# Optimization experiments

Measured on AMD Instinct MI355X. Metric: run time of the kernel, lower is better.

Reference implementation:

```python
import jax, jax.numpy as jnp
import numpy as np

DIM = 64
IN_CH = 3 * DIM          # 192
HID_CH = 2 * IN_CH       # 384
BN_EPS = 1e-5


def setup_inputs() -> dict:
    key = jax.random.key(0)
    ks = jax.random.split(key, 6)
    B, H, W = 8, 256, 256
    x = jax.random.normal(ks[0], (B, H, W, DIM), dtype=jnp.float32)
    gamma = jnp.ones((IN_CH,), dtype=jnp.float32)
    beta = jnp.zeros((IN_CH,), dtype=jnp.float32)
    w_in = jax.random.normal(ks[1], (HID_CH, IN_CH), dtype=jnp.float32) * (1.0 / np.sqrt(IN_CH))
    w_dw = jax.random.normal(ks[2], (HID_CH, 1, 3, 3), dtype=jnp.float32) * (1.0 / 3.0)
    w_out = jax.random.normal(ks[3], (IN_CH, HID_CH), dtype=jnp.float32) * (1.0 / np.sqrt(HID_CH))
    res_scale = jnp.ones((1,), dtype=jnp.float32)
    return {"x": x, "gamma": gamma, "beta": beta, "w_in": w_in,
            "w_dw": w_dw, "w_out": w_out, "res_scale": res_scale}


def _dwt(xc):
    # xc: (B, C, H, W) NCHW, H and W even. Haar via strided slices.
    B, C, H, W = xc.shape
    a = xc[:, :, 0::2, 0::2]
    b = xc[:, :, 0::2, 1::2]
    c = xc[:, :, 1::2, 0::2]
    d = xc[:, :, 1::2, 1::2]
    LLc = (a + b + c + d) * 0.5
    LHc = (a - b + c - d) * 0.5
    HLc = (a + b - c - d) * 0.5
    HHc = (a - b - c + d) * 0.5
    # torch grouped conv output channel order is (channel, subband) flattened,
    # then chunk(4) splits contiguously -> each chunk mixes subbands. Replicate.
    y = jnp.stack([LLc, LHc, HLc, HHc], axis=2)        # (B, C, 4, h, w)
    y = y.reshape(B, 4 * C, H // 2, W // 2)
    return y[:, 0*C:1*C], y[:, 1*C:2*C], y[:, 2*C:3*C], y[:, 3*C:4*C]


def _iwt(LL, LH, HL, HH):
    B, C, h, w = LL.shape
    # cat along channels then view(B,4,C,h,w): interprets as (4, C) layout.
    x4 = jnp.concatenate([LL, LH, HL, HH], axis=1).reshape(B, 4, C, h, w)
    # out[b,c,2p+r,2q+s] = x4[b, 2r+s, c, p, q]
    arr = x4.transpose(0, 2, 1, 3, 4).reshape(B, C, 2, 2, h, w)
    out = arr.transpose(0, 1, 4, 2, 5, 3).reshape(B, C, 2 * h, 2 * w)
    return out


def _mlp(high, gamma, beta, w_in, w_dw, w_out, res_scale):
    # BatchNorm2d in training mode: biased batch stats over (B, H, W)
    mean = jnp.mean(high, axis=(0, 2, 3))
    var = jnp.var(high, axis=(0, 2, 3))
    xn = (high - mean[None, :, None, None]) * jax.lax.rsqrt(var + BN_EPS)[None, :, None, None]
    xn = xn * gamma[None, :, None, None] + beta[None, :, None, None]
    h = jnp.einsum('oc,bchw->bohw', w_in, xn)           # 1x1 conv, no bias
    h = jax.lax.conv_general_dilated(
        h, w_dw, window_strides=(1, 1), padding=((1, 1), (1, 1)),
        dimension_numbers=('NCHW', 'OIHW', 'NCHW'),
        feature_group_count=HID_CH)                      # depthwise 3x3
    h = jax.nn.gelu(h, approximate=False)                # torch nn.GELU default: exact erf
    h = jnp.einsum('oc,bchw->bohw', w_out, h)            # 1x1 conv, no bias
    return high + res_scale[0] * h


def reference(x, gamma, beta, w_in, w_dw, w_out, res_scale):
    xc = jnp.transpose(x, (0, 3, 1, 2))                  # NHWC -> NCHW
    LL, LH, HL, HH = _dwt(xc)
    high = jnp.concatenate([LH, HL, HH], axis=1)         # (B, 3C, h, w)
    high_enh = _mlp(high, gamma, beta, w_in, w_dw, w_out, res_scale)
    C = LL.shape[1]
    LHo, HLo, HHo = high_enh[:, :C], high_enh[:, C:2*C], high_enh[:, 2*C:]
    out = _iwt(LL, LHo, HLo, HHo)                        # (B, C, H, W)
    return jnp.transpose(out, (0, 2, 3, 1))              # back to NHWC
```

## Files before the change

### kernel.cpp

```cpp
#include <hip/hip_runtime.h>
#include <math.h>

typedef unsigned short u16;
typedef unsigned int u32;
typedef __attribute__((ext_vector_type(4))) float f4;
typedef __attribute__((ext_vector_type(2))) float f2;
typedef __attribute__((ext_vector_type(4))) u16 u16x4;
typedef __attribute__((ext_vector_type(8))) u16 u16x8;
typedef __attribute__((ext_vector_type(8))) short bf8;

#define N_IMG 8
#define HS 128
#define NPOS (N_IMG*HS*HS)
#define IN_CH 192
#define HID_CH 384

__device__ __forceinline__ u16 f2bf(float f) {
  union { float f; u32 u; } v; v.f = f;
  u32 r = v.u + 0x7FFFu + ((v.u >> 16) & 1u);
  return (u16)(r >> 16);
}
__device__ __forceinline__ float bf2f(u16 u) {
  union { u32 u; float f; } v; v.u = ((u32)u) << 16; return v.f;
}
__device__ __forceinline__ f2 bfpair(u32 d) {
  union { u32 u; float f; } lo, hi;
  lo.u = d << 16; hi.u = d & 0xffff0000u;
  f2 r; r[0] = lo.f; r[1] = hi.f; return r;
}
__device__ __forceinline__ float gelu_fast(float x) {
  float x2 = x * x;
  float z = x * (-2.302208f - 0.102942f * x2);
  float e = __builtin_amdgcn_exp2f(z);
  return x * __builtin_amdgcn_rcpf(1.0f + e);
}
__device__ __forceinline__ void gl_lds16(const u16* g, u16* l) {
  __builtin_amdgcn_global_load_lds(
      (__attribute__((address_space(1))) void*)(u16*)g,
      (__attribute__((address_space(3))) void*)l, 16, 0, 0);
}

__global__ void k0_zero(float* stats) { stats[threadIdx.x] = 0.0f; }

__global__ __launch_bounds__(256) void k1_dwt(
    const float* __restrict__ x,
    u16* __restrict__ high,
    float* __restrict__ out,
    float* __restrict__ stats)
{
  const int blk = blockIdx.x;
  const int b = blk >> 8, i = (blk >> 1) & 127, jh = blk & 1;
  const int t = threadIdx.x;
  const int c4 = t & 15;
  const int j0 = t >> 4;
  const int jbase = jh * 64 + j0;
  const int rowE = ((b * 256 + 2 * i) * 256) * 64;
  const int rowO = rowE + 256 * 64;
  const bool isHigh = (c4 >= 4);

  float sacc[16], qacc[16];
#pragma unroll
  for (int v = 0; v < 16; v++) { sacc[v] = 0.f; qacc[v] = 0.f; }

  f4 R[2][4];
  {
    const int colE = (2 * jbase) * 64 + c4 * 4;
    R[0][0] = *(const f4*)(x + rowE + colE);
    R[0][1] = *(const f4*)(x + rowE + colE + 64);
    R[0][2] = *(const f4*)(x + rowO + colE);
    R[0][3] = *(const f4*)(x + rowO + colE + 64);
  }

#pragma unroll
  for (int iter = 0; iter < 4; ++iter) {
    const int cur = iter & 1, nxt = cur ^ 1;
    if (iter < 3) {
      const int jn = jbase + 16 * (iter + 1);
      const int colE = (2 * jn) * 64 + c4 * 4;
      R[nxt][0] = *(const f4*)(x + rowE + colE);
      R[nxt][1] = *(const f4*)(x + rowE + colE + 64);
      R[nxt][2] = *(const f4*)(x + rowO + colE);
      R[nxt][3] = *(const f4*)(x + rowO + colE + 64);
    }
    const int j = jbase + 16 * iter;
    f4 va = R[cur][0], vb = R[cur][1], vc = R[cur][2], vd = R[cur][3];
    f4 sb0 = (va + vb + vc + vd) * 0.5f;
    f4 sb1 = (va - vb + vc - vd) * 0.5f;
    f4 sb2 = (va + vb - vc - vd) * 0.5f;
    f4 sb3 = (va - vb - vc + vd) * 0.5f;

    if (!isHigh) {
      float* dst = out + rowE + (2 * j) * 64 + 16 * c4;
#pragma unroll
      for (int cc = 0; cc < 4; cc++) {
        f4 ov;
        ov[0] = sb0[cc]; ov[1] = sb1[cc]; ov[2] = sb2[cc]; ov[3] = sb3[cc];
        ((f4*)dst)[cc] = ov;
      }
    } else {
      const int n = b * 16384 + i * 128 + j;
      u16* dst = high + n * 192 + 16 * (c4 - 4);
#pragma unroll
      for (int half = 0; half < 2; half++) {
        u16x8 pk;
#pragma unroll
        for (int cc2 = 0; cc2 < 2; cc2++) {
          const int cc = half * 2 + cc2;
          pk[cc2 * 4 + 0] = f2bf(sb0[cc]);
          pk[cc2 * 4 + 1] = f2bf(sb1[cc]);
          pk[cc2 * 4 + 2] = f2bf(sb2[cc]);
          pk[cc2 * 4 + 3] = f2bf(sb3[cc]);
        }
        *(u16x8*)(dst + half * 8) = pk;
      }
#pragma unroll
      for (int cc = 0; cc < 4; cc++) {
        float e0 = sb0[cc], e1 = sb1[cc], e2 = sb2[cc], e3 = sb3[cc];
        sacc[cc * 4 + 0] += e0; qacc[cc * 4 + 0] += e0 * e0;
        sacc[cc * 4 + 1] += e1; qacc[cc * 4 + 1] += e1 * e1;
        sacc[cc * 4 + 2] += e2; qacc[cc * 4 + 2] += e2 * e2;
        sacc[cc * 4 + 3] += e3; qacc[cc * 4 + 3] += e3 * e3;
      }
    }
  }

  float vals[32];
#pragma unroll
  for (int v = 0; v < 16; v++) { vals[v] = sacc[v]; vals[16 + v] = qacc[v]; }
#pragma unroll
  for (int v = 0; v < 32; v++) {
    float xx = vals[v];
    xx += __shfl_down(xx, 32);
    xx += __shfl_down(xx, 16);
    vals[v] = xx;
  }
  __shared__ float sred[4][12][32];
  const int lane = t & 63, wave = t >> 6;
  if (lane >= 4 && lane < 16) {
#pragma unroll
    for (int v = 0; v < 32; v++) sred[wave][lane - 4][v] = vals[v];
  }
  __syncthreads();
  if (t < 192) {
    const int g = t >> 4, L = t & 15;
    float s = sred[0][g][L] + sred[1][g][L] + sred[2][g][L] + sred[3][g][L];
    float q = sred[0][g][16 + L] + sred[1][g][16 + L] + sred[2][g][16 + L] + sred[3][g][16 + L];
    atomicAdd(&stats[t], s);
    atomicAdd(&stats[192 + t], q);
  }
}

__global__ void k2a(const float* __restrict__ stats, const float* __restrict__ gamma,
                    const float* __restrict__ beta, float* __restrict__ st)
{
  const int t = threadIdx.x;
  if (t < 192) {
    const float inv_n = 1.0f / 131072.0f;
    float mean = stats[t] * inv_n;
    float var = stats[192 + t] * inv_n - mean * mean;
    var = fmaxf(var, 0.0f);
    float s = gamma[t] * rsqrtf(var + 1e-5f);
    st[t] = s;
    st[192 + t] = beta[t] - mean * s;
  }
}

__global__ __launch_bounds__(64) void k2b(
    const float* __restrict__ w_in, const float* __restrict__ w_out,
    const float* __restrict__ st, const float* __restrict__ res_scale,
    u16* __restrict__ w_in_f, float* __restrict__ bias1, u16* __restrict__ w_out_f)
{
  const int o = blockIdx.x, lane = threadIdx.x;
  if (o < 384) {
    float p = 0.f;
    for (int c = lane; c < 192; c += 64) {
      float w = w_in[o * 192 + c];
      w_in_f[o * 192 + c] = f2bf(w * st[c]);
      p += w * st[192 + c];
    }
#pragma unroll
    for (int off = 32; off; off >>= 1) p += __shfl_down(p, off);
    if (lane == 0) bias1[o] = p;
  } else {
    const int o2 = o - 384;
    const float rs = res_scale[0];
    for (int c = lane; c < 384; c += 64)
      w_out_f[o2 * 384 + c] = f2bf(w_out[o2 * 384 + c] * rs);
  }
}

__global__ __launch_bounds__(256) void k3_gemm1(
    const u16* __restrict__ A,
    const u16* __restrict__ Bw,
    const float* __restrict__ bias,
    u16* __restrict__ C,
    int Mg)
{
  __shared__ __align__(16) u16 smem[128 * 136];
  u16* As = smem;
  u16* Bs = smem + 128 * 32;
  const int t = threadIdx.x;
  const int lane = t & 63, wave = t >> 6;
  const int wm = wave >> 1, wn = wave & 1;
  const int m0 = blockIdx.x * 128;
  const int n0 = blockIdx.y * 128;
  const int lrow = lane >> 2, lcol = lane & 3;
  const int frow = lane & 15, fk = (lane >> 4) * 8;

  f4 acc[4][4];
#pragma unroll
  for (int a = 0; a < 4; a++)
#pragma unroll
    for (int b = 0; b < 4; b++) acc[a][b] = 0.0f;

  for (int ks = 0; ks < 6; ++ks) {
    const int kb = ks * 32;
#pragma unroll
    for (int l = 0; l < 2; ++l) {
      const int r = wave * 32 + l * 16 + lrow;
      gl_lds16(A + (size_t)(m0 + r) * 192 + kb + lcol * 8, As + (wave * 32 + l * 16) * 32);
      gl_lds16(Bw + (size_t)(n0 + r) * 192 + kb + lcol * 8, Bs + (wave * 32 + l * 16) * 32);
    }
    __syncthreads();
    bf8 af[4], bfr[4];
#pragma unroll
    for (int fm = 0; fm < 4; ++fm)
      af[fm] = *(const bf8*)(As + (wm * 64 + fm * 16 + frow) * 32 + fk);
#pragma unroll
    for (int fn = 0; fn < 4; ++fn)
      bfr[fn] = *(const bf8*)(Bs + (wn * 64 + fn * 16 + frow) * 32 + fk);
#pragma unroll
    for (int fm = 0; fm < 4; ++fm)
#pragma unroll
      for (int fn = 0; fn < 4; ++fn)
        acc[fm][fn] = __builtin_amdgcn_mfma_f32_16x16x32_bf16(af[fm], bfr[fn], acc[fm][fn], 0, 0, 0);
    __syncthreads();
  }

  u16* Ct = smem;
  const int r0 = (lane >> 4) * 4, cc = lane & 15;
#pragma unroll
  for (int fn = 0; fn < 4; ++fn) {
    const int ncol = wn * 64 + fn * 16 + cc;
    const float bv = bias[n0 + ncol];
#pragma unroll
    for (int fm = 0; fm < 4; ++fm) {
      const int mr = wm * 64 + fm * 16 + r0;
#pragma unroll
      for (int r = 0; r < 4; ++r)
        Ct[(mr + r) * 136 + ncol] = f2bf(acc[fm][fn][r] + bv);
    }
  }
  __syncthreads();
#pragma unroll
  for (int it = 0; it < 8; ++it) {
    const int idx = it * 256 + t;
    const int row = idx >> 4, seg = idx & 15;
    const int col = n0 + seg * 8;
    const int hsel = (col >= 192) ? 1 : 0;
    u16x8 v = *(const u16x8*)(Ct + row * 136 + seg * 8);
    *(u16x8*)(C + (size_t)hsel * Mg * 192 + (size_t)(m0 + row) * 192 + (col - hsel * 192)) = v;
  }
}

__global__ __launch_bounds__(192) void k4_dw(
    const u16* __restrict__ h1,
    const float* __restrict__ wdw,
    u16* __restrict__ h2,
    int Mg)
{
  const int bx = blockIdx.x;
  const int half = bx & 1;
  const int jt = (bx >> 1) & 15;
  const int rt = (bx >> 5) & 15;
  const int img = bx >> 9;
  const int t = threadIdx.x;
  const int lane = t & 63, wave = t >> 6;
  const int ibase = img * 16384;
  const int r0 = rt * 8;
  const int jBase = (jt == 0) ? 0 : (jt * 8 - 1);
  const int jOff = (jt == 0) ? 0 : 1;
  const size_t hs = (size_t)half * Mg * 192;
  const u16* src = h1 + hs;
  u16* dst = h2 + hs;

  __shared__ u16 lds[10 * 2048];

  for (int i = wave; i < 40; i += 3) {
    const int r = i >> 2, seg = i & 3;
    const int gr = r0 - 1 + r;
    if (gr >= 0 && gr < 128) {
      const u16* g = src + (size_t)(ibase + gr * 128 + jBase) * 192 + seg * 512 + lane * 8;
      gl_lds16(g, &lds[r * 2048 + seg * 512]);
    }
  }
  if (rt == 0) {
    for (int c = t; c < 256; c += 192) *(u16x8*)&lds[c * 8] = (u16x8)(0);
  }
  if (rt == 15) {
    for (int c = t; c < 256; c += 192) *(u16x8*)&lds[9 * 2048 + c * 8] = (u16x8)(0);
  }
  __syncthreads();

  const int o = t % 24, jl = t / 24;
  const int jg = jt * 8 + jl;
  const int cl = o * 8;
  const int cg = half * 192 + cl;

  f2 w2[3][3][4];
#pragma unroll
  for (int dy = 0; dy < 3; dy++)
#pragma unroll
    for (int dx = 0; dx < 3; dx++)
#pragma unroll
      for (int p = 0; p < 4; p++) {
        w2[dy][dx][p][0] = wdw[(cg + 2 * p) * 9 + dy * 3 + dx];
        w2[dy][dx][p][1] = wdw[(cg + 2 * p + 1) * 9 + dy * 3 + dx];
      }

  int im = jl - 1 + jOff; if (im < 0) im = 0;
  const int i0 = jl + jOff, ip = jl + 1 + jOff;

  f2 accA[4], accB[4];
#pragma unroll
  for (int p = 0; p < 4; p++) { accA[p] = (f2)(0.f); accB[p] = (f2)(0.f); }

#pragma unroll
  for (int r = 0; r < 10; ++r) {
    u16x8 vm = *(const u16x8*)&lds[r * 2048 + im * 192 + cl];
    u16x8 v0 = *(const u16x8*)&lds[r * 2048 + i0 * 192 + cl];
    u16x8 vp = *(const u16x8*)&lds[r * 2048 + ip * 192 + cl];
    if (jg == 0)   vm = (u16x8)(0);
    if (jg == 127) vp = (u16x8)(0);
    union { u16x8 v; u32 d[4]; } um, u0, up;
    um.v = vm; u0.v = v0; up.v = vp;
    f2 P0[4], P1[4], P2[4];
#pragma unroll
    for (int p = 0; p < 4; p++) {
      const f2 xm = bfpair(um.d[p]);
      const f2 x0 = bfpair(u0.d[p]);
      const f2 xp = bfpair(up.d[p]);
      P0[p] = w2[0][0][p] * xm + w2[0][1][p] * x0 + w2[0][2][p] * xp;
      P1[p] = w2[1][0][p] * xm + w2[1][1][p] * x0 + w2[1][2][p] * xp;
      P2[p] = w2[2][0][p] * xm + w2[2][1][p] * x0 + w2[2][2][p] * xp;
    }
    if (r >= 2) {
      const int orow = r0 + r - 2;
      u16x8 ov;
#pragma unroll
      for (int p = 0; p < 4; p++) {
        f2 g2 = accA[p] + P2[p];
        ov[2 * p]     = f2bf(gelu_fast(g2[0]));
        ov[2 * p + 1] = f2bf(gelu_fast(g2[1]));
      }
      *(u16x8*)(dst + (size_t)(ibase + orow * 128 + jg) * 192 + cl) = ov;
    }
#pragma unroll
    for (int p = 0; p < 4; p++) {
      accA[p] = accB[p] + P1[p];
      accB[p] = P0[p];
    }
  }
}

__global__ __launch_bounds__(256) void k5_gemm2(
    const u16* __restrict__ A,
    const u16* __restrict__ Bw,
    const u16* __restrict__ high,
    float* __restrict__ out,
    int chunkStart, int Mg)
{
  __shared__ __align__(16) float smemF[128 * 68];
  u16* As = (u16*)smemF;
  u16* Bs = (u16*)smemF + 128 * 32;
  const int t = threadIdx.x;
  const int lane = t & 63, wave = t >> 6;
  const int wm = wave >> 1, wn = wave & 1;
  const int m0 = blockIdx.x * 128;
  const int lrow = lane >> 2, lcol = lane & 3;
  const int frow = lane & 15, fk = (lane >> 4) * 8;

  f4 acc[4][6];
#pragma unroll
  for (int a = 0; a < 4; a++)
#pragma unroll
    for (int b = 0; b < 6; b++) acc[a][b] = 0.0f;

  for (int ks = 0; ks < 12; ++ks) {
    const int kb = ks * 32;
    const u16* Ah = A + (ks >= 6 ? (size_t)Mg * 192 : 0) + (kb - (ks >= 6 ? 192 : 0));
#pragma unroll
    for (int l = 0; l < 2; ++l) {
      const int r = wave * 32 + l * 16 + lrow;
      gl_lds16(Ah + (size_t)(m0 + r) * 192 + lcol * 8, As + (wave * 32 + l * 16) * 32);
    }
#pragma unroll
    for (int l = 0; l < 3; ++l) {
      const int rb = wave * 48 + l * 16 + lrow;
      gl_lds16(Bw + (size_t)rb * 384 + kb + lcol * 8, Bs + (wave * 48 + l * 16) * 32);
    }
    __syncthreads();
    bf8 af[4], bfr[6];
#pragma unroll
    for (int fm = 0; fm < 4; ++fm)
      af[fm] = *(const bf8*)(As + (wm * 64 + fm * 16 + frow) * 32 + fk);
#pragma unroll
    for (int fn = 0; fn < 6; ++fn)
      bfr[fn] = *(const bf8*)(Bs + (wn * 96 + fn * 16 + frow) * 32 + fk);
#pragma unroll
    for (int fm = 0; fm < 4; ++fm)
#pragma unroll
      for (int fn = 0; fn < 6; ++fn)
        acc[fm][fn] = __builtin_amdgcn_mfma_f32_16x16x32_bf16(af[fm], bfr[fn], acc[fm][fn], 0, 0, 0);
    __syncthreads();
  }

  float* Stg = smemF;
  const int r0 = (lane >> 4) * 4, ccol = lane & 15;
#pragma unroll
  for (int bsel = 0; bsel < 3; ++bsel) {
    if (bsel) __syncthreads();
#pragma unroll
    for (int fn = 0; fn < 6; ++fn) {
      const int oc = wn * 96 + fn * 16 + ccol;
      if ((oc >> 6) == bsel) {
        const int c = oc & 63;
#pragma unroll
        for (int fm = 0; fm < 4; ++fm) {
          const int jb = wm * 64 + fm * 16 + r0;
#pragma unroll
          for (int r = 0; r < 4; ++r)
            Stg[(jb + r) * 68 + c] = acc[fm][fn][r];
        }
      }
    }
    __syncthreads();
    const int p = (bsel + 1) >> 1, q = (bsel + 1) & 1;
#pragma unroll
    for (int it = 0; it < 2; ++it) {
      const int jr = (t >> 2) + it * 64;
      const int cq = (t & 3) * 16;
      const int np = chunkStart + m0 + jr;
      const int bi = np >> 14, rem = np & 16383, ii = rem >> 7;
      const u16* hp = high + (size_t)np * 192 + bsel * 64 + cq;
      union { u16x8 v; u32 d[4]; } h0, h1;
      h0.v = *(const u16x8*)hp;
      h1.v = *(const u16x8*)(hp + 8);
      const float* sp = Stg + jr * 68 + cq;
      f4 o0 = *(const f4*)sp;
      f4 o1 = *(const f4*)(sp + 4);
      f4 o2 = *(const f4*)(sp + 8);
      f4 o3 = *(const f4*)(sp + 12);
      f2 a0 = bfpair(h0.d[0]), a1 = bfpair(h0.d[1]), a2 = bfpair(h0.d[2]), a3 = bfpair(h0.d[3]);
      f2 b0 = bfpair(h1.d[0]), b1 = bfpair(h1.d[1]), b2 = bfpair(h1.d[2]), b3 = bfpair(h1.d[3]);
      o0[0] += a0[0]; o0[1] += a0[1]; o0[2] += a1[0]; o0[3] += a1[1];
      o1[0] += a2[0]; o1[1] += a2[1]; o1[2] += a3[0]; o1[3] += a3[1];
      o2[0] += b0[0]; o2[1] += b0[1]; o2[2] += b1[0]; o2[3] += b1[1];
      o3[0] += b2[0]; o3[1] += b2[1]; o3[2] += b3[0]; o3[3] += b3[1];
      float* op = out + (size_t)(((bi * 256 + 2 * ii + p) * 256) + (2 * jr + q)) * 64 + cq;
      *(f4*)op       = o0;
      *(f4*)(op + 4) = o1;
      *(f4*)(op + 8) = o2;
      *(f4*)(op + 12)= o3;
    }
  }
}

extern "C" void kernel_launch(void* const* d_in, const int* in_sizes, int n_in,
                              void* d_out, int out_size, void* d_ws, size_t ws_size,
                              hipStream_t stream)
{
  const float* x        = (const float*)d_in[0];
  const float* gamma    = (const float*)d_in[1];
  const float* beta     = (const float*)d_in[2];
  const float* w_in     = (const float*)d_in[3];
  const float* w_dw     = (const float*)d_in[4];
  const float* w_out    = (const float*)d_in[5];
  const float* res_scale= (const float*)d_in[6];
  float* out = (float*)d_out;
  char* ws = (char*)d_ws;

  float* stats   = (float*)ws;
  float* st      = (float*)(ws + 2048);
  float* bias1   = (float*)(ws + 4096);
  u16*   w_in_f  = (u16*)(ws + 8192);
  u16*   w_out_f = (u16*)(ws + 8192 + 147456);
  u16*   high    = (u16*)(ws + (size_t)(1 << 19));
  const size_t off_h1 = (size_t)(1 << 19) + (size_t)NPOS * 192 * 2;
  const size_t imgBytes = (size_t)16384 * 384 * 2;
  int G = 8;
  while (G > 1 && off_h1 + 2 * (size_t)G * imgBytes > ws_size) G >>= 1;
  u16* h1 = (u16*)(ws + off_h1);
  u16* h2 = (u16*)(ws + off_h1 + (size_t)G * imgBytes);

  k0_zero<<<1, 384, 0, stream>>>(stats);
  k1_dwt<<<2048, 256, 0, stream>>>(x, high, out, stats);
  k2a<<<1, 256, 0, stream>>>(stats, gamma, beta, st);
  k2b<<<576, 64, 0, stream>>>(w_in, w_out, st, res_scale, w_in_f, bias1, w_out_f);

  for (int cs = 0; cs < 8; cs += G) {
    const int chunkStart = cs * 16384;
    const int Mg = G * 16384;
    k3_gemm1<<<dim3(Mg / 128, 3), 256, 0, stream>>>(high + (size_t)chunkStart * 192, w_in_f, bias1, h1, Mg);
    k4_dw<<<G * 512, 192, 0, stream>>>(h1, w_dw, h2, Mg);
    k5_gemm2<<<dim3(Mg / 128, 1), 256, 0, stream>>>(h2, w_out_f, high, out, chunkStart, Mg);
  }
}
```

Measured before the change: 412.5 us.

## Fuse depthwise conv + GELU into second GEMM, removing h2 intermediate

Merges the depthwise 3x3 conv and GELU into the second 1x1 GEMM kernel. Each workgroup loads a 3-row halo slice of h1 per K-step into LDS, computes the depthwise conv and GELU there, and feeds the result straight to the MFMA A tile. Depthwise weights are pre-packed by the prep kernel. This removes the write and re-read of the h2 buffer and a kernel launch, and halves workspace need. In exchange, h1 rows are re-read three times per output row, LDS use rises, and workgroup blocks are remapped in a swizzled order.

Measured after the change: 400.3 us. 3.0% less time.

```diff
diff --git a/kernel.cpp b/kernel.cpp
--- a/kernel.cpp
+++ b/kernel.cpp
@@ -168,7 +168,9 @@
 __global__ __launch_bounds__(64) void k2b(
     const float* __restrict__ w_in, const float* __restrict__ w_out,
     const float* __restrict__ st, const float* __restrict__ res_scale,
-    u16* __restrict__ w_in_f, float* __restrict__ bias1, u16* __restrict__ w_out_f)
+    const float* __restrict__ wdw,
+    u16* __restrict__ w_in_f, float* __restrict__ bias1, u16* __restrict__ w_out_f,
+    float* __restrict__ wdw_pk)
 {
   const int o = blockIdx.x, lane = threadIdx.x;
   if (o < 384) {
@@ -181,11 +183,17 @@
 #pragma unroll
     for (int off = 32; off; off >>= 1) p += __shfl_down(p, off);
     if (lane == 0) bias1[o] = p;
-  } else {
+  } else if (o < 576) {
     const int o2 = o - 384;
     const float rs = res_scale[0];
     for (int c = lane; c < 384; c += 64)
       w_out_f[o2 * 384 + c] = f2bf(w_out[o2 * 384 + c] * rs);
+  } else {
+    const int oct = o - 576;
+    for (int q = lane; q < 72; q += 64) {
+      const int tap = q >> 3, e = q & 7;
+      wdw_pk[oct * 72 + q] = wdw[(oct * 8 + e) * 9 + tap];
+    }
   }
 }
 
@@ -263,136 +271,61 @@
   }
 }
 
-__global__ __launch_bounds__(192) void k4_dw(
+__global__ __launch_bounds__(256) void k45_dwgemm2(
     const u16* __restrict__ h1,
-    const float* __restrict__ wdw,
-    u16* __restrict__ h2,
-    int Mg)
-{
-  const int bx = blockIdx.x;
-  const int half = bx & 1;
-  const int jt = (bx >> 1) & 15;
-  const int rt = (bx >> 5) & 15;
-  const int img = bx >> 9;
-  const int t = threadIdx.x;
-  const int lane = t & 63, wave = t >> 6;
-  const int ibase = img * 16384;
-  const int r0 = rt * 8;
-  const int jBase = (jt == 0) ? 0 : (jt * 8 - 1);
-  const int jOff = (jt == 0) ? 0 : 1;
-  const size_t hs = (size_t)half * Mg * 192;
-  const u16* src = h1 + hs;
-  u16* dst = h2 + hs;
-
-  __shared__ u16 lds[10 * 2048];
-
-  for (int i = wave; i < 40; i += 3) {
-    const int r = i >> 2, seg = i & 3;
-    const int gr = r0 - 1 + r;
-    if (gr >= 0 && gr < 128) {
-      const u16* g = src + (size_t)(ibase + gr * 128 + jBase) * 192 + seg * 512 + lane * 8;
-      gl_lds16(g, &lds[r * 2048 + seg * 512]);
-    }
-  }
-  if (rt == 0) {
-    for (int c = t; c < 256; c += 192) *(u16x8*)&lds[c * 8] = (u16x8)(0);
-  }
-  if (rt == 15) {
-    for (int c = t; c < 256; c += 192) *(u16x8*)&lds[9 * 2048 + c * 8] = (u16x8)(0);
-  }
-  __syncthreads();
-
-  const int o = t % 24, jl = t / 24;
-  const int jg = jt * 8 + jl;
-  const int cl = o * 8;
-  const int cg = half * 192 + cl;
-
-  f2 w2[3][3][4];
-#pragma unroll
-  for (int dy = 0; dy < 3; dy++)
-#pragma unroll
-    for (int dx = 0; dx < 3; dx++)
-#pragma unroll
-      for (int p = 0; p < 4; p++) {
-        w2[dy][dx][p][0] = wdw[(cg + 2 * p) * 9 + dy * 3 + dx];
-        w2[dy][dx][p][1] = wdw[(cg + 2 * p + 1) * 9 + dy * 3 + dx];
-      }
-
-  int im = jl - 1 + jOff; if (im < 0) im = 0;
-  const int i0 = jl + jOff, ip = jl + 1 + jOff;
-
-  f2 accA[4], accB[4];
-#pragma unroll
-  for (int p = 0; p < 4; p++) { accA[p] = (f2)(0.f); accB[p] = (f2)(0.f); }
-
-#pragma unroll
-  for (int r = 0; r < 10; ++r) {
-    u16x8 vm = *(const u16x8*)&lds[r * 2048 + im * 192 + cl];
-    u16x8 v0 = *(const u16x8*)&lds[r * 2048 + i0 * 192 + cl];
-    u16x8 vp = *(const u16x8*)&lds[r * 2048 + ip * 192 + cl];
-    if (jg == 0)   vm = (u16x8)(0);
-    if (jg == 127) vp = (u16x8)(0);
-    union { u16x8 v; u32 d[4]; } um, u0, up;
-    um.v = vm; u0.v = v0; up.v = vp;
-    f2 P0[4], P1[4], P2[4];
-#pragma unroll
-    for (int p = 0; p < 4; p++) {
-      const f2 xm = bfpair(um.d[p]);
-      const f2 x0 = bfpair(u0.d[p]);
-      const f2 xp = bfpair(up.d[p]);
-      P0[p] = w2[0][0][p] * xm + w2[0][1][p] * x0 + w2[0][2][p] * xp;
-      P1[p] = w2[1][0][p] * xm + w2[1][1][p] * x0 + w2[1][2][p] * xp;
-      P2[p] = w2[2][0][p] * xm + w2[2][1][p] * x0 + w2[2][2][p] * xp;
-    }
-    if (r >= 2) {
-      const int orow = r0 + r - 2;
-      u16x8 ov;
-#pragma unroll
-      for (int p = 0; p < 4; p++) {
-        f2 g2 = accA[p] + P2[p];
-        ov[2 * p]     = f2bf(gelu_fast(g2[0]));
-        ov[2 * p + 1] = f2bf(gelu_fast(g2[1]));
-      }
-      *(u16x8*)(dst + (size_t)(ibase + orow * 128 + jg) * 192 + cl) = ov;
-    }
-#pragma unroll
-    for (int p = 0; p < 4; p++) {
-      accA[p] = accB[p] + P1[p];
-      accB[p] = P0[p];
-    }
-  }
-}
-
-__global__ __launch_bounds__(256) void k5_gemm2(
-    const u16* __restrict__ A,
+    const float* __restrict__ wdw_pk,
     const u16* __restrict__ Bw,
     const u16* __restrict__ high,
     float* __restrict__ out,
     int chunkStart, int Mg)
 {
-  __shared__ __align__(16) float smemF[128 * 68];
-  u16* As = (u16*)smemF;
-  u16* Bs = (u16*)smemF + 128 * 32;
+  __shared__ __align__(16) char smem_raw[13824 + 45056];
+  float* wlds = (float*)smem_raw;
+  u16* h1t = (u16*)(smem_raw + 13824);
+  u16* Asl = (u16*)(smem_raw + 13824 + 24576);
+  u16* Bs  = (u16*)(smem_raw + 13824 + 24576 + 8192);
+  float* Stg = (float*)(smem_raw + 13824);
+
   const int t = threadIdx.x;
   const int lane = t & 63, wave = t >> 6;
   const int wm = wave >> 1, wn = wave & 1;
-  const int m0 = blockIdx.x * 128;
+  const int nwg = gridDim.x;
+  const int wg = (blockIdx.x & 7) * (nwg >> 3) + (blockIdx.x >> 3);
+  const int img = wg >> 7, irow = wg & 127;
+  const int m0 = wg * 128;
   const int lrow = lane >> 2, lcol = lane & 3;
   const int frow = lane & 15, fk = (lane >> 4) * 8;
 
+  for (int q = t; q < 3456; q += 256) wlds[q] = wdw_pk[q];
+  if (irow == 0) {
+    for (int q = t; q < 512; q += 256) *(u16x8*)(h1t + q * 8) = (u16x8)(0);
+  }
+  if (irow == 127) {
+    for (int q = t; q < 512; q += 256) *(u16x8*)(h1t + 2 * 4096 + q * 8) = (u16x8)(0);
+  }
+
   f4 acc[4][6];
 #pragma unroll
   for (int a = 0; a < 4; a++)
 #pragma unroll
     for (int b = 0; b < 6; b++) acc[a][b] = 0.0f;
+
+  const int oct = t & 3, j0q = t >> 2;
 
   for (int ks = 0; ks < 12; ++ks) {
     const int kb = ks * 32;
-    const u16* Ah = A + (ks >= 6 ? (size_t)Mg * 192 : 0) + (kb - (ks >= 6 ? 192 : 0));
-#pragma unroll
-    for (int l = 0; l < 2; ++l) {
-      const int r = wave * 32 + l * 16 + lrow;
-      gl_lds16(Ah + (size_t)(m0 + r) * 192 + lcol * 8, As + (wave * 32 + l * 16) * 32);
+    const int half = (ks >= 6) ? 1 : 0;
+    const int klocal = kb - half * 192;
+    const u16* hsrc = h1 + (size_t)half * Mg * 192 + klocal;
+
+    for (int is = wave; is < 24; is += 4) {
+      const int dy = is >> 3, seg = is & 7;
+      const int gr = irow - 1 + dy;
+      if (gr >= 0 && gr < 128) {
+        const int j = seg * 16 + (lane >> 2);
+        gl_lds16(hsrc + (size_t)(img * 16384 + gr * 128 + j) * 192 + (lane & 3) * 8,
+                 h1t + (dy * 128 + seg * 16) * 32);
+      }
     }
 #pragma unroll
     for (int l = 0; l < 3; ++l) {
@@ -400,10 +333,56 @@
       gl_lds16(Bw + (size_t)rb * 384 + kb + lcol * 8, Bs + (wave * 48 + l * 16) * 32);
     }
     __syncthreads();
+
+    f4 w4[9][2];
+    {
+      const float* wp = wlds + (ks * 4 + oct) * 72;
+#pragma unroll
+      for (int tap = 0; tap < 9; ++tap) {
+        w4[tap][0] = *(const f4*)(wp + tap * 8);
+        w4[tap][1] = *(const f4*)(wp + tap * 8 + 4);
+      }
+    }
+#pragma unroll
+    for (int jj2 = 0; jj2 < 2; ++jj2) {
+      const int jj = j0q + jj2 * 64;
+      f2 accd[4];
+#pragma unroll
+      for (int p = 0; p < 4; p++) accd[p] = (f2)(0.f);
+#pragma unroll
+      for (int dy = 0; dy < 3; ++dy) {
+        const int base = (dy * 128 + jj) * 32 + oct * 8;
+        u16x8 xc = *(const u16x8*)(h1t + base);
+        u16x8 xl = (jj != 0)   ? *(const u16x8*)(h1t + base - 32) : (u16x8)(0);
+        u16x8 xr = (jj != 127) ? *(const u16x8*)(h1t + base + 32) : (u16x8)(0);
+        union { u16x8 v; u32 d[4]; } ul, uc, ur;
+        ul.v = xl; uc.v = xc; ur.v = xr;
+#pragma unroll
+        for (int p = 0; p < 4; p++) {
+          f2 wl, wc, wr;
+          wl[0] = w4[dy * 3 + 0][p >> 1][2 * (p & 1)];
+          wl[1] = w4[dy * 3 + 0][p >> 1][2 * (p & 1) + 1];
+          wc[0] = w4[dy * 3 + 1][p >> 1][2 * (p & 1)];
+          wc[1] = w4[dy * 3 + 1][p >> 1][2 * (p & 1) + 1];
+          wr[0] = w4[dy * 3 + 2][p >> 1][2 * (p & 1)];
+          wr[1] = w4[dy * 3 + 2][p >> 1][2 * (p & 1) + 1];
+          accd[p] += wl * bfpair(ul.d[p]) + wc * bfpair(uc.d[p]) + wr * bfpair(ur.d[p]);
+        }
+      }
+      u16x8 ov;
+#pragma unroll
+      for (int p = 0; p < 4; p++) {
+        ov[2 * p]     = f2bf(gelu_fast(accd[p][0]));
+        ov[2 * p + 1] = f2bf(gelu_fast(accd[p][1]));
+      }
+      *(u16x8*)(Asl + jj * 32 + oct * 8) = ov;
+    }
+    __syncthreads();
+
     bf8 af[4], bfr[6];
 #pragma unroll
     for (int fm = 0; fm < 4; ++fm)
-      af[fm] = *(const bf8*)(As + (wm * 64 + fm * 16 + frow) * 32 + fk);
+      af[fm] = *(const bf8*)(Asl + (wm * 64 + fm * 16 + frow) * 32 + fk);
 #pragma unroll
     for (int fn = 0; fn < 6; ++fn)
       bfr[fn] = *(const bf8*)(Bs + (wn * 96 + fn * 16 + frow) * 32 + fk);
@@ -415,7 +394,6 @@
     __syncthreads();
   }
 
-  float* Stg = smemF;
   const int r0 = (lane >> 4) * 4, ccol = lane & 15;
 #pragma unroll
   for (int bsel = 0; bsel < 3; ++bsel) {
@@ -443,16 +421,16 @@
       const int np = chunkStart + m0 + jr;
       const int bi = np >> 14, rem = np & 16383, ii = rem >> 7;
       const u16* hp = high + (size_t)np * 192 + bsel * 64 + cq;
-      union { u16x8 v; u32 d[4]; } h0, h1;
+      union { u16x8 v; u32 d[4]; } h0, h1u;
       h0.v = *(const u16x8*)hp;
-      h1.v = *(const u16x8*)(hp + 8);
+      h1u.v = *(const u16x8*)(hp + 8);
       const float* sp = Stg + jr * 68 + cq;
       f4 o0 = *(const f4*)sp;
       f4 o1 = *(const f4*)(sp + 4);
       f4 o2 = *(const f4*)(sp + 8);
       f4 o3 = *(const f4*)(sp + 12);
       f2 a0 = bfpair(h0.d[0]), a1 = bfpair(h0.d[1]), a2 = bfpair(h0.d[2]), a3 = bfpair(h0.d[3]);
-      f2 b0 = bfpair(h1.d[0]), b1 = bfpair(h1.d[1]), b2 = bfpair(h1.d[2]), b3 = bfpair(h1.d[3]);
+      f2 b0 = bfpair(h1u.d[0]), b1 = bfpair(h1u.d[1]), b2 = bfpair(h1u.d[2]), b3 = bfpair(h1u.d[3]);
       o0[0] += a0[0]; o0[1] += a0[1]; o0[2] += a1[0]; o0[3] += a1[1];
       o1[0] += a2[0]; o1[1] += a2[1]; o1[2] += a3[0]; o1[3] += a3[1];
       o2[0] += b0[0]; o2[1] += b0[1]; o2[2] += b1[0]; o2[3] += b1[1];
@@ -485,24 +463,23 @@
   float* bias1   = (float*)(ws + 4096);
   u16*   w_in_f  = (u16*)(ws + 8192);
   u16*   w_out_f = (u16*)(ws + 8192 + 147456);
+  float* wdw_pk  = (float*)(ws + 8192 + 2 * 147456);
   u16*   high    = (u16*)(ws + (size_t)(1 << 19));
   const size_t off_h1 = (size_t)(1 << 19) + (size_t)NPOS * 192 * 2;
   const size_t imgBytes = (size_t)16384 * 384 * 2;
   int G = 8;
-  while (G > 1 && off_h1 + 2 * (size_t)G * imgBytes > ws_size) G >>= 1;
+  while (G > 1 && off_h1 + (size_t)G * imgBytes > ws_size) G >>= 1;
   u16* h1 = (u16*)(ws + off_h1);
-  u16* h2 = (u16*)(ws + off_h1 + (size_t)G * imgBytes);
 
   k0_zero<<<1, 384, 0, stream>>>(stats);
   k1_dwt<<<2048, 256, 0, stream>>>(x, high, out, stats);
   k2a<<<1, 256, 0, stream>>>(stats, gamma, beta, st);
-  k2b<<<576, 64, 0, stream>>>(w_in, w_out, st, res_scale, w_in_f, bias1, w_out_f);
+  k2b<<<624, 64, 0, stream>>>(w_in, w_out, st, res_scale, w_dw, w_in_f, bias1, w_out_f, wdw_pk);
 
   for (int cs = 0; cs < 8; cs += G) {
     const int chunkStart = cs * 16384;
     const int Mg = G * 16384;
     k3_gemm1<<<dim3(Mg / 128, 3), 256, 0, stream>>>(high + (size_t)chunkStart * 192, w_in_f, bias1, h1, Mg);
-    k4_dw<<<G * 512, 192, 0, stream>>>(h1, w_dw, h2, Mg);
-    k5_gemm2<<<dim3(Mg / 128, 1), 256, 0, stream>>>(h2, w_out_f, high, out, chunkStart, Mg);
-  }
-}
+    k45_dwgemm2<<<G * 128, 256, 0, stream>>>(h1, wdw_pk, w_out_f, high, out, chunkStart, Mg);
+  }
+}
```
